# Kernel optimization log

Hardware: AMD Instinct MI355X
Metric: run time of the kernel (lower is better)

The kernel has to match this reference:

```python
import jax, jax.numpy as jnp
import numpy as np

B, S, D, H = 4, 2048, 1024, 16
HD = D // H  # head_dim = 64


def setup_inputs() -> dict:
    key = jax.random.key(0)
    ks = jax.random.split(key, 5)
    scale = 1.0 / np.sqrt(D)
    return {
        "x": jax.random.normal(ks[0], (B, S, D), dtype=jnp.float32),
        "Wq": jax.random.normal(ks[1], (D, D), dtype=jnp.float32) * scale,
        "bq": jnp.zeros((D,), dtype=jnp.float32),
        "Wk": jax.random.normal(ks[2], (D, D), dtype=jnp.float32) * scale,
        "bk": jnp.zeros((D,), dtype=jnp.float32),
        "Wv": jax.random.normal(ks[3], (D, D), dtype=jnp.float32) * scale,
        "bv": jnp.zeros((D,), dtype=jnp.float32),
        "Wo": jax.random.normal(ks[4], (D, D), dtype=jnp.float32) * scale,
        "bo": jnp.zeros((D,), dtype=jnp.float32),
    }


def reference(x, Wq, bq, Wk, bk, Wv, bv, Wo, bo):
    # Linear layers (torch Linear: y = x @ W^T + b)
    q = jnp.einsum("bsd,ed->bse", x, Wq) + bq
    k = jnp.einsum("bsd,ed->bse", x, Wk) + bk
    v = jnp.einsum("bsd,ed->bse", x, Wv) + bv
    # split heads -> [B, H, S, HD]
    q = q.reshape(B, S, H, HD).transpose(0, 2, 1, 3)
    k = k.reshape(B, S, H, HD).transpose(0, 2, 1, 3)
    v = v.reshape(B, S, H, HD).transpose(0, 2, 1, 3)
    # NOTE: original scales by 1/sqrt(d_model), not 1/sqrt(head_dim)
    scores = jnp.einsum("bhqd,bhkd->bhqk", q, k) / jnp.sqrt(jnp.float32(D))
    causal = jnp.tril(jnp.ones((S, S), dtype=bool))
    scores = jnp.where(causal, scores, -jnp.inf)
    probs = jax.nn.softmax(scores, axis=-1)  # dropout p=0 -> identity
    attn = jnp.einsum("bhqk,bhkd->bhqd", probs, v)
    # merge heads -> [B, S, D]
    attn = attn.transpose(0, 2, 1, 3).reshape(B, S, D)
    out = jnp.einsum("bsd,ed->bse", attn, Wo) + bo
    return out
```

## Files before the change

### kernel.cpp

```cpp
#include <hip/hip_runtime.h>
#include <hip/hip_bf16.h>
#include <stdint.h>
#include <stddef.h>

#define B_N 4
#define S_N 2048
#define D_N 1024
#define H_N 16
#define HD_N 64

typedef __bf16 bf16;
typedef __bf16 bf16x8 __attribute__((ext_vector_type(8)));
typedef __bf16 bf16x4 __attribute__((ext_vector_type(4)));
typedef float f32x4 __attribute__((ext_vector_type(4)));

__device__ __forceinline__ void gload_lds16(const void* g, void* l) {
  __builtin_amdgcn_global_load_lds((const __attribute__((address_space(1))) void*)g,
                                   (__attribute__((address_space(3))) void*)l,
                                   16, 0, 0);
}

__global__ __launch_bounds__(256) void cvt_f32_bf16(const float* __restrict__ in,
                                                    bf16* __restrict__ out, int n4) {
  int i = blockIdx.x * blockDim.x + threadIdx.x;
  const int stride = gridDim.x * blockDim.x;
  for (; i < n4; i += stride) {
    const float4 v = ((const float4*)in)[i];
    bf16x4 o;
    o[0] = (bf16)v.x; o[1] = (bf16)v.y; o[2] = (bf16)v.z; o[3] = (bf16)v.w;
    ((bf16x4*)out)[i] = o;
  }
}

__global__ __launch_bounds__(256) void cvt_w4(const float* __restrict__ w0,
                                              const float* __restrict__ w1,
                                              const float* __restrict__ w2,
                                              const float* __restrict__ w3,
                                              bf16* __restrict__ o0, bf16* __restrict__ o1,
                                              bf16* __restrict__ o2, bf16* __restrict__ o3) {
  const int n4 = (D_N * D_N) / 4;
  const int which = blockIdx.x >> 9;
  const float* in = which == 0 ? w0 : which == 1 ? w1 : which == 2 ? w2 : w3;
  bf16* out = which == 0 ? o0 : which == 1 ? o1 : which == 2 ? o2 : o3;
  int i = (blockIdx.x & 511) * 256 + threadIdx.x;
  const int stride = 512 * 256;
  for (; i < n4; i += stride) {
    const float4 v = ((const float4*)in)[i];
    bf16x4 o;
    o[0] = (bf16)v.x; o[1] = (bf16)v.y; o[2] = (bf16)v.z; o[3] = (bf16)v.w;
    ((bf16x4*)out)[i] = o;
  }
}

template <typename OutFn>
__device__ __forceinline__ void gemm_body(const bf16* __restrict__ A,
                                          const bf16* __restrict__ W, int m0, int n0,
                                          bf16* sA, bf16* sB, OutFn&& emit) {
  const int tid = threadIdx.x;
  const int wave = tid >> 6;
  const int lane = tid & 63;
  const int l16 = lane & 15;
  const int lhi = lane >> 4;
  const int wm = (wave >> 1) * 64;
  const int wn = (wave & 1) * 64;
  const int rA = lane >> 2;
  const int cA = (lane & 3) * 8;

  const f32x4 z4 = {0.0f, 0.0f, 0.0f, 0.0f};
  f32x4 acc[4][4];
#pragma unroll
  for (int i = 0; i < 4; ++i)
#pragma unroll
    for (int j = 0; j < 4; ++j) acc[i][j] = z4;

  for (int k0 = 0; k0 < D_N; k0 += 32) {
#pragma unroll
    for (int is = 0; is < 2; ++is) {
      const int r = is * 64 + wave * 16;
      gload_lds16(A + (size_t)(m0 + r + rA) * D_N + k0 + cA, &sA[r * 32]);
      gload_lds16(W + (size_t)(n0 + r + rA) * D_N + k0 + cA, &sB[r * 32]);
    }
    __syncthreads();
    bf16x8 af[4], bfr[4];
#pragma unroll
    for (int i = 0; i < 4; ++i)
      af[i] = *(const bf16x8*)&sA[(wm + i * 16 + l16) * 32 + lhi * 8];
#pragma unroll
    for (int j = 0; j < 4; ++j)
      bfr[j] = *(const bf16x8*)&sB[(wn + j * 16 + l16) * 32 + lhi * 8];
#pragma unroll
    for (int i = 0; i < 4; ++i)
#pragma unroll
      for (int j = 0; j < 4; ++j)
        acc[i][j] = __builtin_amdgcn_mfma_f32_16x16x32_bf16(af[i], bfr[j], acc[i][j], 0, 0, 0);
    __syncthreads();
  }
#pragma unroll
  for (int i = 0; i < 4; ++i)
#pragma unroll
    for (int j = 0; j < 4; ++j)
      emit(m0 + wm + i * 16 + lhi * 4, n0 + wn + j * 16 + l16, acc[i][j]);
}

__global__ __launch_bounds__(256) void gemm_qkv(const bf16* __restrict__ A,
                                                const bf16* __restrict__ Wq,
                                                const bf16* __restrict__ Wk,
                                                const bf16* __restrict__ Wv,
                                                const float* __restrict__ bq,
                                                const float* __restrict__ bk,
                                                const float* __restrict__ bv,
                                                bf16* __restrict__ outQ,
                                                bf16* __restrict__ outK,
                                                bf16* __restrict__ outVt) {
  __shared__ bf16 sA[128 * 32];
  __shared__ bf16 sB[128 * 32];
  const int which = blockIdx.x >> 3;
  const int n0 = (blockIdx.x & 7) * 128;
  const int m0 = blockIdx.y * 128;
  const bf16* W = which == 0 ? Wq : which == 1 ? Wk : Wv;
  const float* bias = which == 0 ? bq : which == 1 ? bk : bv;

  if (which == 2) {
    gemm_body(A, W, m0, n0, sA, sB, [&](int row0, int col, const f32x4& a) {
      const float bvv = bias[col];
      const int b = row0 >> 11, s = row0 & (S_N - 1);
      const int h = col >> 6, hd = col & 63;
      bf16x4 pk;
#pragma unroll
      for (int r = 0; r < 4; ++r) pk[r] = (bf16)(a[r] + bvv);
      *(bf16x4*)&outVt[(((size_t)b * H_N + h) * HD_N + hd) * S_N + s] = pk;
    });
  } else {
    bf16* out = which == 0 ? outQ : outK;
    gemm_body(A, W, m0, n0, sA, sB, [&](int row0, int col, const f32x4& a) {
      const float bvv = bias[col];
      const int h = col >> 6, hd = col & 63;
#pragma unroll
      for (int r = 0; r < 4; ++r) {
        const int row = row0 + r;
        const int b = row >> 11, s = row & (S_N - 1);
        out[(((size_t)b * H_N + h) * S_N + s) * HD_N + hd] = (bf16)(a[r] + bvv);
      }
    });
  }
}

__global__ __launch_bounds__(256) void gemm_out(const bf16* __restrict__ A,
                                                const bf16* __restrict__ W,
                                                const float* __restrict__ bias,
                                                float* __restrict__ out) {
  __shared__ bf16 sA[128 * 32];
  __shared__ bf16 sB[128 * 32];
  const int n0 = blockIdx.x * 128;
  const int m0 = blockIdx.y * 128;
  gemm_body(A, W, m0, n0, sA, sB, [&](int row0, int col, const f32x4& a) {
    const float bvv = bias[col];
#pragma unroll
    for (int r = 0; r < 4; ++r) out[(size_t)(row0 + r) * D_N + col] = a[r] + bvv;
  });
}

__global__ __launch_bounds__(256, 3) void attn_fwd(const bf16* __restrict__ Q,
                                                   const bf16* __restrict__ K,
                                                   const bf16* __restrict__ Vt,
                                                   bf16* __restrict__ O) {
  __shared__ __align__(16) bf16 sK[2][64 * 64];
  __shared__ __align__(16) bf16 sV[2][64 * 64];
  __shared__ __align__(16) bf16 sP[4][32 * 72];
  const int tid = threadIdx.x;
  const int wave = tid >> 6;
  const int lane = tid & 63;
  const int l16 = lane & 15;
  const int lhi = lane >> 4;
  const int bidx = blockIdx.x;
  const int bh = bidx & 63;
  const int qt = 15 - (bidx >> 6);
  const int q0 = qt * 128 + wave * 32;
  const bf16* Qh = Q + (size_t)bh * S_N * HD_N;
  const bf16* Kh = K + (size_t)bh * S_N * HD_N;
  const bf16* Vth = Vt + (size_t)bh * HD_N * S_N;
  const int b = bh >> 4, h = bh & 15;

  const int srow = lane >> 3;
  const int scol = 8 * ((lane & 7) ^ srow);

  const float QS = 0.03125f * 1.44269504088896340736f;
  const f32x4 z4 = {0.0f, 0.0f, 0.0f, 0.0f};
  const f32x4 m4 = {-4.0f, -4.0f, -4.0f, -4.0f};
  const bf16 oneb = (bf16)1.0f;
  const bf16x8 ones = {oneb, oneb, oneb, oneb, oneb, oneb, oneb, oneb};
  bf16* sPw = sP[wave];

  bf16x8 qf[2][2];
#pragma unroll
  for (int i = 0; i < 2; ++i)
#pragma unroll
    for (int kq = 0; kq < 2; ++kq) {
      const bf16x8 raw =
          *(const bf16x8*)&Qh[(size_t)(q0 + i * 16 + l16) * HD_N + kq * 32 + lhi * 8];
      bf16x8 s;
#pragma unroll
      for (int e = 0; e < 8; ++e) s[e] = (bf16)((float)raw[e] * QS);
      qf[i][kq] = s;
    }

  f32x4 o[2][4];
  f32x4 osum[2];
#pragma unroll
  for (int i = 0; i < 2; ++i) {
#pragma unroll
    for (int j = 0; j < 4; ++j) o[i][j] = z4;
    osum[i] = z4;
  }

#define STAGE(buf, kb_)                                                                  \
  {                                                                                      \
    _Pragma("unroll") for (int is = 0; is < 2; ++is) {                                   \
      const int r0 = is * 32 + wave * 8;                                                 \
      gload_lds16(Kh + (size_t)((kb_)*64 + r0 + srow) * HD_N + scol, &sK[buf][r0 * 64]); \
      gload_lds16(Vth + (size_t)(r0 + srow) * S_N + (kb_)*64 + scol, &sV[buf][r0 * 64]); \
    }                                                                                    \
  }

  const int nkb = 2 * qt + 2;

  STAGE(0, 0);
  __syncthreads();

  for (int kb = 0; kb < nkb; ++kb) {
    const int cur = kb & 1;
    if (kb + 1 < nkb) STAGE(cur ^ 1, kb + 1);
    const bf16* sKb = sK[cur];
    const bf16* sVb = sV[cur];
    const int k0 = kb * 64;

    if (k0 <= q0 + 31) {
      f32x4 sc[2][4];
#pragma unroll
      for (int i = 0; i < 2; ++i)
#pragma unroll
        for (int j = 0; j < 4; ++j) sc[i][j] = m4;
      __builtin_amdgcn_s_setprio(1);
#pragma unroll
      for (int j = 0; j < 4; ++j) {
        const int row = j * 16 + l16;
#pragma unroll
        for (int kq = 0; kq < 2; ++kq) {
          const bf16x8 kfr = *(const bf16x8*)((const char*)sKb + row * 128 +
                                              ((kq * 64 + lhi * 16) ^ ((row & 7) << 4)));
#pragma unroll
          for (int i = 0; i < 2; ++i)
            sc[i][j] = __builtin_amdgcn_mfma_f32_16x16x32_bf16(qf[i][kq], kfr, sc[i][j], 0, 0, 0);
        }
      }
      __builtin_amdgcn_s_setprio(0);

      if (k0 + 63 > q0) {
#pragma unroll
        for (int i = 0; i < 2; ++i)
#pragma unroll
          for (int r = 0; r < 4; ++r) {
            const int qrow = q0 + i * 16 + lhi * 4 + r;
#pragma unroll
            for (int j = 0; j < 4; ++j)
              if (k0 + j * 16 + l16 > qrow) sc[i][j][r] = -3e38f;
          }
      }

#pragma unroll
      for (int i = 0; i < 2; ++i)
#pragma unroll
        for (int r = 0; r < 4; ++r)
#pragma unroll
          for (int j = 0; j < 4; ++j)
            sPw[(i * 16 + lhi * 4 + r) * 72 + j * 16 + l16] = (bf16)__builtin_exp2f(sc[i][j][r]);

      __builtin_amdgcn_s_setprio(1);
#pragma unroll
      for (int kq = 0; kq < 2; ++kq) {
        bf16x8 pa[2];
#pragma unroll
        for (int i = 0; i < 2; ++i)
          pa[i] = *(const bf16x8*)&sPw[(i * 16 + l16) * 72 + kq * 32 + lhi * 8];
#pragma unroll
        for (int i = 0; i < 2; ++i)
          osum[i] = __builtin_amdgcn_mfma_f32_16x16x32_bf16(pa[i], ones, osum[i], 0, 0, 0);
#pragma unroll
        for (int jd = 0; jd < 4; ++jd) {
          const int vrow = jd * 16 + l16;
          const bf16x8 vb = *(const bf16x8*)((const char*)sVb + vrow * 128 +
                                             ((kq * 64 + lhi * 16) ^ ((vrow & 7) << 4)));
#pragma unroll
          for (int i = 0; i < 2; ++i)
            o[i][jd] = __builtin_amdgcn_mfma_f32_16x16x32_bf16(pa[i], vb, o[i][jd], 0, 0, 0);
        }
      }
      __builtin_amdgcn_s_setprio(0);
    }
    __syncthreads();
  }

#pragma unroll
  for (int i = 0; i < 2; ++i) {
#pragma unroll
    for (int r = 0; r < 4; ++r) {
      const float inv = 1.0f / osum[i][r];
      const size_t token = (size_t)b * S_N + q0 + i * 16 + lhi * 4 + r;
#pragma unroll
      for (int jd = 0; jd < 4; ++jd) {
        const int col = h * 64 + jd * 16 + l16;
        O[token * D_N + col] = (bf16)(o[i][jd][r] * inv);
      }
    }
  }
#undef STAGE
}

extern "C" void kernel_launch(void* const* d_in, const int* in_sizes, int n_in,
                              void* d_out, int out_size, void* d_ws, size_t ws_size,
                              hipStream_t stream) {
  const float* x  = (const float*)d_in[0];
  const float* Wq = (const float*)d_in[1];
  const float* bq = (const float*)d_in[2];
  const float* Wk = (const float*)d_in[3];
  const float* bk = (const float*)d_in[4];
  const float* Wv = (const float*)d_in[5];
  const float* bv = (const float*)d_in[6];
  const float* Wo = (const float*)d_in[7];
  const float* bo = (const float*)d_in[8];

  char* ws = (char*)d_ws;
  const size_t MB = 1u << 20;
  bf16* xb  = (bf16*)(ws);
  bf16* qB  = (bf16*)(ws + 16 * MB);
  bf16* kB  = (bf16*)(ws + 32 * MB);
  bf16* vtB = (bf16*)(ws + 48 * MB);
  bf16* wqb = (bf16*)(ws + 64 * MB);
  bf16* wkb = (bf16*)(ws + 66 * MB);
  bf16* wvb = (bf16*)(ws + 68 * MB);
  bf16* wob = (bf16*)(ws + 70 * MB);

  cvt_f32_bf16<<<2048, 256, 0, stream>>>(x, xb, (B_N * S_N * D_N) / 4);
  cvt_w4<<<2048, 256, 0, stream>>>(Wq, Wk, Wv, Wo, wqb, wkb, wvb, wob);

  gemm_qkv<<<dim3(24, (B_N * S_N) / 128), 256, 0, stream>>>(xb, wqb, wkb, wvb, bq, bk, bv,
                                                            qB, kB, vtB);

  attn_fwd<<<dim3(1024), 256, 0, stream>>>(qB, kB, vtB, xb);

  gemm_out<<<dim3(D_N / 128, (B_N * S_N) / 128), 256, 0, stream>>>(xb, wob, bo, (float*)d_out);
}
```

Measured before the change: 183.9 us.

## Triple-buffer GEMM with swizzled LDS, 256x128 tiles, and 512-thread blocks

Rewrites the shared GEMM body used by the QKV and output projections. It now uses a three-stage software pipeline with K=64 steps, so global-to-LDS loads for tile t+2 overlap the MFMA work on tile t. The LDS layout gets an XOR swizzle to avoid bank conflicts. The block tile grows to 256x128 with 8 waves, and MFMA sections get raised wave priority. Each block uses about 147KB of LDS, which limits occupancy to one block per CU. The loop also depends on hand-written vmcnt and barrier sequencing being correct.

```diff
diff --git a/kernel.cpp b/kernel.cpp
--- a/kernel.cpp
+++ b/kernel.cpp
@@ -55,7 +55,7 @@
 template <typename OutFn>
 __device__ __forceinline__ void gemm_body(const bf16* __restrict__ A,
                                           const bf16* __restrict__ W, int m0, int n0,
-                                          bf16* sA, bf16* sB, OutFn&& emit) {
+                                          bf16* sAq, bf16* sBq, OutFn&& emit) {
   const int tid = threadIdx.x;
   const int wave = tid >> 6;
   const int lane = tid & 63;
@@ -63,38 +63,73 @@
   const int lhi = lane >> 4;
   const int wm = (wave >> 1) * 64;
   const int wn = (wave & 1) * 64;
-  const int rA = lane >> 2;
-  const int cA = (lane & 3) * 8;
-
-  const f32x4 z4 = {0.0f, 0.0f, 0.0f, 0.0f};
+  const int srow = wave * 8 + (lane >> 3);
+  const int scol = 8 * ((lane & 7) ^ (lane >> 3));
+  const int sdst = wave * 8 * 64;
+  const int aoff0 = (lhi ^ (l16 & 7)) * 8;
+
   f32x4 acc[4][4];
 #pragma unroll
   for (int i = 0; i < 4; ++i)
 #pragma unroll
-    for (int j = 0; j < 4; ++j) acc[i][j] = z4;
-
-  for (int k0 = 0; k0 < D_N; k0 += 32) {
-#pragma unroll
-    for (int is = 0; is < 2; ++is) {
-      const int r = is * 64 + wave * 16;
-      gload_lds16(A + (size_t)(m0 + r + rA) * D_N + k0 + cA, &sA[r * 32]);
-      gload_lds16(W + (size_t)(n0 + r + rA) * D_N + k0 + cA, &sB[r * 32]);
-    }
-    __syncthreads();
-    bf16x8 af[4], bfr[4];
-#pragma unroll
-    for (int i = 0; i < 4; ++i)
-      af[i] = *(const bf16x8*)&sA[(wm + i * 16 + l16) * 32 + lhi * 8];
-#pragma unroll
-    for (int j = 0; j < 4; ++j)
-      bfr[j] = *(const bf16x8*)&sB[(wn + j * 16 + l16) * 32 + lhi * 8];
-#pragma unroll
-    for (int i = 0; i < 4; ++i)
-#pragma unroll
-      for (int j = 0; j < 4; ++j)
-        acc[i][j] = __builtin_amdgcn_mfma_f32_16x16x32_bf16(af[i], bfr[j], acc[i][j], 0, 0, 0);
-    __syncthreads();
-  }
+    for (int j = 0; j < 4; ++j) acc[i][j] = (f32x4){0.f, 0.f, 0.f, 0.f};
+
+#define SG_A(buf_, kt_)                                                                 \
+  {                                                                                     \
+    _Pragma("unroll") for (int q = 0; q < 4; ++q)                                       \
+        gload_lds16(A + (size_t)(m0 + q * 64 + srow) * D_N + (kt_) * 64 + scol,         \
+                    sAq + (buf_) * 16384 + sdst + q * 4096);                            \
+  }
+#define SG_B(buf_, kt_)                                                                 \
+  {                                                                                     \
+    _Pragma("unroll") for (int q = 0; q < 2; ++q)                                       \
+        gload_lds16(W + (size_t)(n0 + q * 64 + srow) * D_N + (kt_) * 64 + scol,         \
+                    sBq + (buf_) * 8192 + sdst + q * 4096);                             \
+  }
+#define PHASE(cur_, kk_)                                                                \
+  {                                                                                     \
+    const bf16* a_ = sAq + (cur_) * 16384;                                              \
+    const bf16* b_ = sBq + (cur_) * 8192;                                               \
+    bf16x8 af[4], bfr[4];                                                               \
+    _Pragma("unroll") for (int i = 0; i < 4; ++i)                                       \
+        af[i] = *(const bf16x8*)(a_ + (wm + i * 16 + l16) * 64 + (aoff0 ^ ((kk_)*32))); \
+    _Pragma("unroll") for (int j = 0; j < 4; ++j)                                       \
+        bfr[j] = *(const bf16x8*)(b_ + (wn + j * 16 + l16) * 64 + (aoff0 ^ ((kk_)*32)));\
+    __builtin_amdgcn_s_setprio(1);                                                      \
+    _Pragma("unroll") for (int i = 0; i < 4; ++i)                                       \
+        _Pragma("unroll") for (int j = 0; j < 4; ++j)                                   \
+            acc[i][j] = __builtin_amdgcn_mfma_f32_16x16x32_bf16(af[i], bfr[j],          \
+                                                                acc[i][j], 0, 0, 0);    \
+    __builtin_amdgcn_s_setprio(0);                                                      \
+  }
+
+  const int NT = D_N / 64;
+
+  SG_A(0, 0); SG_B(0, 0);
+  SG_A(1, 1); SG_B(1, 1);
+  asm volatile("s_waitcnt vmcnt(6)" ::: "memory");
+  asm volatile("s_barrier" ::: "memory");
+
+  for (int t = 0; t < NT - 2; ++t) {
+    const int cur = t % 3, nx = (t + 2) % 3;
+    SG_A(nx, t + 2);
+    PHASE(cur, 0);
+    SG_B(nx, t + 2);
+    PHASE(cur, 1);
+    asm volatile("s_waitcnt vmcnt(6) lgkmcnt(0)" ::: "memory");
+    asm volatile("s_barrier" ::: "memory");
+  }
+  PHASE((NT - 2) % 3, 0);
+  PHASE((NT - 2) % 3, 1);
+  asm volatile("s_waitcnt vmcnt(0) lgkmcnt(0)" ::: "memory");
+  asm volatile("s_barrier" ::: "memory");
+  PHASE((NT - 1) % 3, 0);
+  PHASE((NT - 1) % 3, 1);
+
+#undef SG_A
+#undef SG_B
+#undef PHASE
+
 #pragma unroll
   for (int i = 0; i < 4; ++i)
 #pragma unroll
@@ -102,7 +137,7 @@
       emit(m0 + wm + i * 16 + lhi * 4, n0 + wn + j * 16 + l16, acc[i][j]);
 }
 
-__global__ __launch_bounds__(256) void gemm_qkv(const bf16* __restrict__ A,
+__global__ __launch_bounds__(512) void gemm_qkv(const bf16* __restrict__ A,
                                                 const bf16* __restrict__ Wq,
                                                 const bf16* __restrict__ Wk,
                                                 const bf16* __restrict__ Wv,
@@ -112,16 +147,16 @@
                                                 bf16* __restrict__ outQ,
                                                 bf16* __restrict__ outK,
                                                 bf16* __restrict__ outVt) {
-  __shared__ bf16 sA[128 * 32];
-  __shared__ bf16 sB[128 * 32];
+  __shared__ __align__(16) bf16 sAq[3 * 256 * 64];
+  __shared__ __align__(16) bf16 sBq[3 * 128 * 64];
   const int which = blockIdx.x >> 3;
   const int n0 = (blockIdx.x & 7) * 128;
-  const int m0 = blockIdx.y * 128;
+  const int m0 = blockIdx.y * 256;
   const bf16* W = which == 0 ? Wq : which == 1 ? Wk : Wv;
   const float* bias = which == 0 ? bq : which == 1 ? bk : bv;
 
   if (which == 2) {
-    gemm_body(A, W, m0, n0, sA, sB, [&](int row0, int col, const f32x4& a) {
+    gemm_body(A, W, m0, n0, sAq, sBq, [&](int row0, int col, const f32x4& a) {
       const float bvv = bias[col];
       const int b = row0 >> 11, s = row0 & (S_N - 1);
       const int h = col >> 6, hd = col & 63;
@@ -132,7 +167,7 @@
     });
   } else {
     bf16* out = which == 0 ? outQ : outK;
-    gemm_body(A, W, m0, n0, sA, sB, [&](int row0, int col, const f32x4& a) {
+    gemm_body(A, W, m0, n0, sAq, sBq, [&](int row0, int col, const f32x4& a) {
       const float bvv = bias[col];
       const int h = col >> 6, hd = col & 63;
 #pragma unroll
@@ -145,15 +180,15 @@
   }
 }
 
-__global__ __launch_bounds__(256) void gemm_out(const bf16* __restrict__ A,
+__global__ __launch_bounds__(512) void gemm_out(const bf16* __restrict__ A,
                                                 const bf16* __restrict__ W,
                                                 const float* __restrict__ bias,
                                                 float* __restrict__ out) {
-  __shared__ bf16 sA[128 * 32];
-  __shared__ bf16 sB[128 * 32];
+  __shared__ __align__(16) bf16 sAq[3 * 256 * 64];
+  __shared__ __align__(16) bf16 sBq[3 * 128 * 64];
   const int n0 = blockIdx.x * 128;
-  const int m0 = blockIdx.y * 128;
-  gemm_body(A, W, m0, n0, sA, sB, [&](int row0, int col, const f32x4& a) {
+  const int m0 = blockIdx.y * 256;
+  gemm_body(A, W, m0, n0, sAq, sBq, [&](int row0, int col, const f32x4& a) {
     const float bvv = bias[col];
 #pragma unroll
     for (int r = 0; r < 4; ++r) out[(size_t)(row0 + r) * D_N + col] = a[r] + bvv;
@@ -343,10 +378,9 @@
   cvt_f32_bf16<<<2048, 256, 0, stream>>>(x, xb, (B_N * S_N * D_N) / 4);
   cvt_w4<<<2048, 256, 0, stream>>>(Wq, Wk, Wv, Wo, wqb, wkb, wvb, wob);
 
-  gemm_qkv<<<dim3(24, (B_N * S_N) / 128), 256, 0, stream>>>(xb, wqb, wkb, wvb, bq, bk, bv,
-                                                            qB, kB, vtB);
+  gemm_qkv<<<dim3(24, 32), 512, 0, stream>>>(xb, wqb, wkb, wvb, bq, bk, bv, qB, kB, vtB);
 
   attn_fwd<<<dim3(1024), 256, 0, stream>>>(qB, kB, vtB, xb);
 
-  gemm_out<<<dim3(D_N / 128, (B_N * S_N) / 128), 256, 0, stream>>>(xb, wob, bo, (float*)d_out);
-}
+  gemm_out<<<dim3(8, 32), 512, 0, stream>>>(xb, wob, bo, (float*)d_out);
+}
```

After: 188.9 us. 1.03x slower.
